# Optimization experiments

Hardware: AMD Instinct MI355X
Metric: run time of the kernel (lower is better)

## Reference

```python
import jax, jax.numpy as jnp
import numpy as np

TEMPERATURE = 1.0

def _cauchy_kernel(x, y, temperature):
    # pairwise squared distances via Gram trick: ||x_i - y_j||^2
    sq_x = jnp.sum(x * x, axis=1)  # [n]
    sq_y = jnp.sum(y * y, axis=1)  # [m]
    d2 = sq_x[:, None] + sq_y[None, :] - 2.0 * (x @ y.T)
    d2 = jnp.maximum(d2, 0.0)
    return 1.0 / (1.0 + d2 / temperature)


def setup_inputs() -> dict:
    key = jax.random.key(0)
    k1, k2 = jax.random.split(key)
    features = jax.random.normal(k1, (8192, 128), dtype=jnp.float32)
    labels = jax.random.randint(k2, (8192,), 0, 1000, dtype=jnp.int64)
    return {"features": features, "labels": labels}


def reference(features, labels):
    b = features.shape[0] // 2
    z1 = features[:b]
    z2 = features[b:]
    z11 = _cauchy_kernel(z1, z1, TEMPERATURE)  # [b,b]
    z22 = _cauchy_kernel(z2, z2, TEMPERATURE)  # [b,b]
    z12 = _cauchy_kernel(z1, z2, TEMPERATURE)  # [b,b]

    eye = jnp.eye(b, dtype=z11.dtype)
    # positive term: mean log of matched-pair kernel (diagonal of z12)
    pos = jnp.sum(jnp.log(jnp.diagonal(z12))) / b
    # negative terms: row sums over [z11 - I | z12] and [z12^T | z22 - I]
    n1 = jnp.mean(jnp.log((z11 - eye).sum(axis=1) + z12.sum(axis=1)))
    n2 = jnp.mean(jnp.log(z12.sum(axis=0) + (z22 - eye).sum(axis=1)))
    neg = (n1 + n2) / 2.0
    return -(pos - neg)
```

## Files before the change

kernel.cpp:

```cpp
#include <hip/hip_runtime.h>
#include <math.h>

#define N_TOTAL 8192
#define BHALF   4096
#define KDIM    128
#define NTILE   64
#define NBLK    512

typedef __bf16 bf16x8 __attribute__((ext_vector_type(8)));
typedef __bf16 bf16x2 __attribute__((ext_vector_type(2)));
typedef float  f32x4  __attribute__((ext_vector_type(4)));

#define GLOAD_LDS16(GSRC, LDST)                                                \
    __builtin_amdgcn_global_load_lds(                                          \
        (const __attribute__((address_space(1))) void*)(GSRC),                 \
        (__attribute__((address_space(3))) void*)(LDST), 16, 0, 0)

__global__ __launch_bounds__(256) void k_prep_pos(const float* __restrict__ F,
                                                  __bf16* __restrict__ Fbf,
                                                  float* __restrict__ sq,
                                                  float* __restrict__ posPart,
                                                  float* __restrict__ out) {
    int t = threadIdx.x;
    int w = t >> 6, l = t & 63;
    int p = blockIdx.x * 4 + w;
    const float2* r1 = (const float2*)(F + (size_t)p * KDIM);
    const float2* r2 = (const float2*)(F + (size_t)(p + BHALF) * KDIM);
    float2 a = r1[l];
    float2 c = r2[l];

    float s1 = fmaf(a.x, a.x, a.y * a.y);
    float s2 = fmaf(c.x, c.x, c.y * c.y);
    float dp = fmaf(a.x, c.x, a.y * c.y);
#pragma unroll
    for (int off = 32; off > 0; off >>= 1) {
        s1 += __shfl_down(s1, off);
        s2 += __shfl_down(s2, off);
        dp += __shfl_down(dp, off);
    }

    bf16x2 pa, pc;
    pa[0] = (__bf16)a.x; pa[1] = (__bf16)a.y;
    pc[0] = (__bf16)c.x; pc[1] = (__bf16)c.y;
    ((bf16x2*)(Fbf + (size_t)p * KDIM))[l] = pa;
    ((bf16x2*)(Fbf + (size_t)(p + BHALF) * KDIM))[l] = pc;

    __shared__ float posRed[4];
    if (l == 0) {
        sq[p] = s1;
        sq[p + BHALF] = s2;
        float d2 = fmaxf(s1 + s2 - 2.0f * dp, 0.0f);
        posRed[w] = logf(1.0f + d2);
    }
    __syncthreads();
    if (t == 0) {
        posPart[blockIdx.x] = posRed[0] + posRed[1] + posRed[2] + posRed[3];
        if (blockIdx.x == 0) out[0] = 0.0f;
    }
}

__global__ __launch_bounds__(512, 4) void k_pairwise(
        const __bf16* __restrict__ Fbf,
        const float* __restrict__ sq,
        float* __restrict__ Tpart) {
    __shared__ __align__(16) __bf16 As[128 * 128];
    __shared__ __align__(16) __bf16 Bs[128 * 128];
    __shared__ float rowAcc[128][2];
    __shared__ float colAcc[128][4];

    int t = threadIdx.x;
    int w = t >> 6;
    int l = t & 63;
    int wr = w >> 1, wc = w & 1;
    int low = l & 15, kb = l >> 4;

    int bid = blockIdx.x;
    int start, cnt;
    if (bid < 480) { start = bid * 4;              cnt = 4; }
    else           { start = 1920 + (bid - 480) * 5; cnt = 5; }

    int ti = (int)floorf((129.0f - sqrtf(16641.0f - 8.0f * (float)start)) * 0.5f);
    while (ti * (129 - ti) / 2 > start) --ti;
    while ((ti + 1) * (128 - ti) / 2 <= start) ++ti;
    int tj = ti + (start - ti * (129 - ti) / 2);

    auto stage = [&](const __bf16* src, __bf16* dst) {
#pragma unroll
        for (int it = 0; it < 4; ++it) {
            int f = it * 512 + t;
            int row = f >> 4;
            int sg = f & 15;
            int g = sg ^ (row & 15);
            GLOAD_LDS16(src + row * KDIM + g * 8, dst + (size_t)f * 8);
        }
    };

    stage(Fbf + (size_t)ti * 128 * KDIM, As);
    if (ti != tj) stage(Fbf + (size_t)tj * 128 * KDIM, Bs);
    __syncthreads();

#pragma unroll 1
    for (int n = 0; n < cnt; ++n) {
        int I = ti * 128, J = tj * 128;
        bool diag = (ti == tj);

        const bf16x8* Asg = (const bf16x8*)As;
        const bf16x8* Bsg = diag ? (const bf16x8*)As : (const bf16x8*)Bs;
        f32x4 acc[2][4] = {};
#pragma unroll
        for (int s = 0; s < 4; ++s) {
            int g = s * 4 + kb;
            bf16x8 aF[2], bF[4];
#pragma unroll
            for (int fr = 0; fr < 2; ++fr) {
                int R = wr * 32 + fr * 16 + low;
                aF[fr] = Asg[R * 16 + (g ^ low)];
            }
#pragma unroll
            for (int fc = 0; fc < 4; ++fc) {
                int C = wc * 64 + fc * 16 + low;
                bF[fc] = Bsg[C * 16 + (g ^ low)];
            }
#pragma unroll
            for (int fr = 0; fr < 2; ++fr)
#pragma unroll
                for (int fc = 0; fc < 4; ++fc)
                    acc[fr][fc] = __builtin_amdgcn_mfma_f32_16x16x32_bf16(
                        aF[fr], bF[fc], acc[fr][fc], 0, 0, 0);
        }
        __syncthreads();

        int nti = ti, ntj = tj + 1;
        if (ntj == NTILE) { ++nti; ntj = nti; }
        if (n + 1 < cnt) {
            if (nti != ti)  stage(Fbf + (size_t)nti * 128 * KDIM, As);
            if (nti != ntj) stage(Fbf + (size_t)ntj * 128 * KDIM, Bs);
        }

        float sqi[2][4], sqj[4];
#pragma unroll
        for (int fr = 0; fr < 2; ++fr)
#pragma unroll
            for (int r = 0; r < 4; ++r)
                sqi[fr][r] = sq[I + wr * 32 + fr * 16 + kb * 4 + r];
#pragma unroll
        for (int fc = 0; fc < 4; ++fc)
            sqj[fc] = sq[J + wc * 64 + fc * 16 + low];

        float rowPart[2][4] = {};
        float colPart[4] = {0.f, 0.f, 0.f, 0.f};
#pragma unroll
        for (int fr = 0; fr < 2; ++fr) {
#pragma unroll
            for (int fc = 0; fc < 4; ++fc) {
#pragma unroll
                for (int r = 0; r < 4; ++r) {
                    float d2 = sqi[fr][r] + sqj[fc] - 2.0f * acc[fr][fc][r];
                    d2 = fmaxf(d2, 0.0f);
                    float v = __builtin_amdgcn_rcpf(1.0f + d2);
                    rowPart[fr][r] += v;
                    colPart[fc] += v;
                }
            }
        }

#pragma unroll
        for (int fr = 0; fr < 2; ++fr)
#pragma unroll
            for (int r = 0; r < 4; ++r) {
                float x = rowPart[fr][r];
                x += __shfl_xor(x, 1);
                x += __shfl_xor(x, 2);
                x += __shfl_xor(x, 4);
                x += __shfl_xor(x, 8);
                if (low == 0)
                    rowAcc[wr * 32 + fr * 16 + kb * 4 + r][wc] = x;
            }

#pragma unroll
        for (int fc = 0; fc < 4; ++fc) {
            float x = colPart[fc];
            x += __shfl_xor(x, 16);
            x += __shfl_xor(x, 32);
            if (kb == 0)
                colAcc[wc * 64 + fc * 16 + low][wr] = x;
        }
        __syncthreads();

        if (t < 128) {
            Tpart[tj * N_TOTAL + I + t] = rowAcc[t][0] + rowAcc[t][1];
        } else if (t < 256 && !diag) {
            int c = t - 128;
            Tpart[ti * N_TOTAL + J + c] =
                colAcc[c][0] + colAcc[c][1] + colAcc[c][2] + colAcc[c][3];
        }

        ti = nti; tj = ntj;
    }
}

__global__ __launch_bounds__(256) void k_final(const float* __restrict__ Tpart,
                                               const float* __restrict__ posPart,
                                               float* __restrict__ out) {
    int t = threadIdx.x;
    int i = blockIdx.x * 256 + t;
    float s = 0.0f;
#pragma unroll 8
    for (int k = 0; k < NTILE; ++k) s += Tpart[k * N_TOTAL + i];
    float v = logf(s - 1.0f);
    if (t < 32) v += 2.0f * posPart[blockIdx.x * 32 + t];
#pragma unroll
    for (int off = 32; off > 0; off >>= 1) v += __shfl_down(v, off);
    __shared__ float red[4];
    int w = t >> 6, l = t & 63;
    if (l == 0) red[w] = v;
    __syncthreads();
    if (t == 0) {
        float S = red[0] + red[1] + red[2] + red[3];
        atomicAdd(out, S * (1.0f / (2.0f * (float)BHALF)));
    }
}

extern "C" void kernel_launch(void* const* d_in, const int* in_sizes, int n_in,
                              void* d_out, int out_size, void* d_ws, size_t ws_size,
                              hipStream_t stream) {
    const float* F = (const float*)d_in[0];
    float* out = (float*)d_out;

    char* ws = (char*)d_ws;
    __bf16* Fbf     = (__bf16*)ws;
    float*  sq      = (float*)(ws + (size_t)N_TOTAL * KDIM * 2);
    float*  posPart = sq + N_TOTAL;
    float*  Tpart   = posPart + 1024;

    k_prep_pos<<<BHALF / 4, 256, 0, stream>>>(F, Fbf, sq, posPart, out);
    k_pairwise<<<NBLK, 512, 0, stream>>>(Fbf, sq, Tpart);
    k_final<<<N_TOTAL / 256, 256, 0, stream>>>(Tpart, posPart, out);
}
```

Baseline: 87.53 us.

## Pin A tile in registers per row-chunk and accumulate row sums across tiles

Each block now owns one row tile and up to four consecutive column tiles. The A fragments and row norms are loaded into registers once, and row partial sums are accumulated in registers across the chunk and reduced once at the end. This halves LDS usage by dropping the As buffer, removes per-tile A restaging and row reductions, and can raise occupancy. The prep kernel zeroes Tpart because fewer slots get written, and the grid grows to 544 blocks with uneven work per block.

```diff
diff --git a/kernel.cpp b/kernel.cpp
--- a/kernel.cpp
+++ b/kernel.cpp
@@ -5,7 +5,8 @@
 #define BHALF   4096
 #define KDIM    128
 #define NTILE   64
-#define NBLK    512
+#define NCHUNK  544
+#define NSLOT   64
 
 typedef __bf16 bf16x8 __attribute__((ext_vector_type(8)));
 typedef __bf16 bf16x2 __attribute__((ext_vector_type(2)));
@@ -20,6 +21,7 @@
                                                   __bf16* __restrict__ Fbf,
                                                   float* __restrict__ sq,
                                                   float* __restrict__ posPart,
+                                                  float* __restrict__ Tpart,
                                                   float* __restrict__ out) {
     int t = threadIdx.x;
     int w = t >> 6, l = t & 63;
@@ -29,6 +31,10 @@
     float2 a = r1[l];
     float2 c = r2[l];
 
+    int zi = blockIdx.x * 256 + t;
+    Tpart[zi] = 0.0f;
+    Tpart[zi + 262144] = 0.0f;
+
     float s1 = fmaf(a.x, a.x, a.y * a.y);
     float s2 = fmaf(c.x, c.x, c.y * c.y);
     float dp = fmaf(a.x, c.x, a.y * c.y);
@@ -63,10 +69,9 @@
         const __bf16* __restrict__ Fbf,
         const float* __restrict__ sq,
         float* __restrict__ Tpart) {
-    __shared__ __align__(16) __bf16 As[128 * 128];
-    __shared__ __align__(16) __bf16 Bs[128 * 128];
+    __shared__ __align__(16) __bf16 Bs[128 * KDIM];
+    __shared__ float colAcc[128][4];
     __shared__ float rowAcc[128][2];
-    __shared__ float colAcc[128][4];
 
     int t = threadIdx.x;
     int w = t >> 6;
@@ -75,47 +80,58 @@
     int low = l & 15, kb = l >> 4;
 
     int bid = blockIdx.x;
-    int start, cnt;
-    if (bid < 480) { start = bid * 4;              cnt = 4; }
-    else           { start = 1920 + (bid - 480) * 5; cnt = 5; }
-
-    int ti = (int)floorf((129.0f - sqrtf(16641.0f - 8.0f * (float)start)) * 0.5f);
-    while (ti * (129 - ti) / 2 > start) --ti;
-    while ((ti + 1) * (128 - ti) / 2 <= start) ++ti;
-    int tj = ti + (start - ti * (129 - ti) / 2);
-
-    auto stage = [&](const __bf16* src, __bf16* dst) {
+    int ti = 0, base = 0;
+    for (;;) {
+        int nch = (NTILE - ti + 3) >> 2;
+        if (bid < base + nch) break;
+        base += nch;
+        ++ti;
+    }
+    int c = bid - base;
+    int tj0 = ti + c * 4;
+    int cnt = NTILE - tj0; if (cnt > 4) cnt = 4;
+    int I = ti * 128;
+
+    auto stage = [&](const __bf16* src) {
 #pragma unroll
         for (int it = 0; it < 4; ++it) {
             int f = it * 512 + t;
             int row = f >> 4;
             int sg = f & 15;
             int g = sg ^ (row & 15);
-            GLOAD_LDS16(src + row * KDIM + g * 8, dst + (size_t)f * 8);
+            GLOAD_LDS16(src + row * KDIM + g * 8, Bs + (size_t)f * 8);
         }
     };
 
-    stage(Fbf + (size_t)ti * 128 * KDIM, As);
-    if (ti != tj) stage(Fbf + (size_t)tj * 128 * KDIM, Bs);
+    stage(Fbf + (size_t)tj0 * 128 * KDIM);
+    const __bf16* baseA = Fbf + (size_t)(I + wr * 32 + low) * KDIM + kb * 8;
+    bf16x8 aR[2][4];
+#pragma unroll
+    for (int fr = 0; fr < 2; ++fr)
+#pragma unroll
+        for (int s = 0; s < 4; ++s)
+            aR[fr][s] = *(const bf16x8*)(baseA + fr * 16 * KDIM + s * 32);
+    float sqi[2][4];
+#pragma unroll
+    for (int fr = 0; fr < 2; ++fr)
+#pragma unroll
+        for (int r = 0; r < 4; ++r)
+            sqi[fr][r] = sq[I + wr * 32 + fr * 16 + kb * 4 + r];
+    float rowPartR[2][4] = {};
     __syncthreads();
 
 #pragma unroll 1
     for (int n = 0; n < cnt; ++n) {
-        int I = ti * 128, J = tj * 128;
-        bool diag = (ti == tj);
-
-        const bf16x8* Asg = (const bf16x8*)As;
-        const bf16x8* Bsg = diag ? (const bf16x8*)As : (const bf16x8*)Bs;
+        int tj = tj0 + n;
+        int J = tj * 128;
+        bool diag = (tj == ti);
+
+        const bf16x8* Bsg = (const bf16x8*)Bs;
         f32x4 acc[2][4] = {};
 #pragma unroll
         for (int s = 0; s < 4; ++s) {
             int g = s * 4 + kb;
-            bf16x8 aF[2], bF[4];
-#pragma unroll
-            for (int fr = 0; fr < 2; ++fr) {
-                int R = wr * 32 + fr * 16 + low;
-                aF[fr] = Asg[R * 16 + (g ^ low)];
-            }
+            bf16x8 bF[4];
 #pragma unroll
             for (int fc = 0; fc < 4; ++fc) {
                 int C = wc * 64 + fc * 16 + low;
@@ -126,28 +142,17 @@
 #pragma unroll
                 for (int fc = 0; fc < 4; ++fc)
                     acc[fr][fc] = __builtin_amdgcn_mfma_f32_16x16x32_bf16(
-                        aF[fr], bF[fc], acc[fr][fc], 0, 0, 0);
+                        aR[fr][s], bF[fc], acc[fr][fc], 0, 0, 0);
         }
         __syncthreads();
 
-        int nti = ti, ntj = tj + 1;
-        if (ntj == NTILE) { ++nti; ntj = nti; }
-        if (n + 1 < cnt) {
-            if (nti != ti)  stage(Fbf + (size_t)nti * 128 * KDIM, As);
-            if (nti != ntj) stage(Fbf + (size_t)ntj * 128 * KDIM, Bs);
-        }
-
-        float sqi[2][4], sqj[4];
-#pragma unroll
-        for (int fr = 0; fr < 2; ++fr)
-#pragma unroll
-            for (int r = 0; r < 4; ++r)
-                sqi[fr][r] = sq[I + wr * 32 + fr * 16 + kb * 4 + r];
+        if (n + 1 < cnt) stage(Fbf + (size_t)(tj + 1) * 128 * KDIM);
+
+        float sqj[4];
 #pragma unroll
         for (int fc = 0; fc < 4; ++fc)
             sqj[fc] = sq[J + wc * 64 + fc * 16 + low];
 
-        float rowPart[2][4] = {};
         float colPart[4] = {0.f, 0.f, 0.f, 0.f};
 #pragma unroll
         for (int fr = 0; fr < 2; ++fr) {
@@ -158,24 +163,11 @@
                     float d2 = sqi[fr][r] + sqj[fc] - 2.0f * acc[fr][fc][r];
                     d2 = fmaxf(d2, 0.0f);
                     float v = __builtin_amdgcn_rcpf(1.0f + d2);
-                    rowPart[fr][r] += v;
+                    rowPartR[fr][r] += v;
                     colPart[fc] += v;
                 }
             }
         }
-
-#pragma unroll
-        for (int fr = 0; fr < 2; ++fr)
-#pragma unroll
-            for (int r = 0; r < 4; ++r) {
-                float x = rowPart[fr][r];
-                x += __shfl_xor(x, 1);
-                x += __shfl_xor(x, 2);
-                x += __shfl_xor(x, 4);
-                x += __shfl_xor(x, 8);
-                if (low == 0)
-                    rowAcc[wr * 32 + fr * 16 + kb * 4 + r][wc] = x;
-            }
 
 #pragma unroll
         for (int fc = 0; fc < 4; ++fc) {
@@ -187,15 +179,27 @@
         }
         __syncthreads();
 
-        if (t < 128) {
-            Tpart[tj * N_TOTAL + I + t] = rowAcc[t][0] + rowAcc[t][1];
-        } else if (t < 256 && !diag) {
-            int c = t - 128;
-            Tpart[ti * N_TOTAL + J + c] =
-                colAcc[c][0] + colAcc[c][1] + colAcc[c][2] + colAcc[c][3];
-        }
-
-        ti = nti; tj = ntj;
+        if (!diag && t < 128) {
+            Tpart[ti * N_TOTAL + J + t] =
+                colAcc[t][0] + colAcc[t][1] + colAcc[t][2] + colAcc[t][3];
+        }
+    }
+
+#pragma unroll
+    for (int fr = 0; fr < 2; ++fr)
+#pragma unroll
+        for (int r = 0; r < 4; ++r) {
+            float x = rowPartR[fr][r];
+            x += __shfl_xor(x, 1);
+            x += __shfl_xor(x, 2);
+            x += __shfl_xor(x, 4);
+            x += __shfl_xor(x, 8);
+            if (low == 0)
+                rowAcc[wr * 32 + fr * 16 + kb * 4 + r][wc] = x;
+        }
+    __syncthreads();
+    if (t < 128) {
+        Tpart[(ti + c) * N_TOTAL + I + t] = rowAcc[t][0] + rowAcc[t][1];
     }
 }
 
@@ -206,7 +210,7 @@
     int i = blockIdx.x * 256 + t;
     float s = 0.0f;
 #pragma unroll 8
-    for (int k = 0; k < NTILE; ++k) s += Tpart[k * N_TOTAL + i];
+    for (int k = 0; k < NSLOT; ++k) s += Tpart[k * N_TOTAL + i];
     float v = logf(s - 1.0f);
     if (t < 32) v += 2.0f * posPart[blockIdx.x * 32 + t];
 #pragma unroll
@@ -233,7 +237,7 @@
     float*  posPart = sq + N_TOTAL;
     float*  Tpart   = posPart + 1024;
 
-    k_prep_pos<<<BHALF / 4, 256, 0, stream>>>(F, Fbf, sq, posPart, out);
-    k_pairwise<<<NBLK, 512, 0, stream>>>(Fbf, sq, Tpart);
+    k_prep_pos<<<BHALF / 4, 256, 0, stream>>>(F, Fbf, sq, posPart, Tpart, out);
+    k_pairwise<<<NCHUNK, 512, 0, stream>>>(Fbf, sq, Tpart);
     k_final<<<N_TOTAL / 256, 256, 0, stream>>>(Tpart, posPart, out);
 }
```

Result: slower. 97.27 us (+11.1%).
